# Kernel tuning notes

Measured on AMD Instinct MI355X. Metric: run time of the kernel, lower is better.

Reference implementation:

```python
import jax, jax.numpy as jnp
import numpy as np

B, T, HID = 2, 2048, 2048
NH, NKV = 16, 8
NOPE, ROPE = 128, 64
HD = NOPE + ROPE  # 192
VD = 128
KV_RANK, Q_RANK = 512, 1536
EPS = 1e-6
THETA = 10000.0
GROUPS = NH // NKV


def rmsnorm(x, w):
    var = jnp.mean(x * x, axis=-1, keepdims=True)
    return x * jax.lax.rsqrt(var + EPS) * w


def rope_cos_sin(seq_len, dtype):
    inv_freq = 1.0 / (THETA ** (jnp.arange(0, ROPE, 2, dtype=jnp.float32) / ROPE))
    t = jnp.arange(seq_len, dtype=jnp.float32)
    freqs = jnp.outer(t, inv_freq)
    emb = jnp.concatenate([freqs, freqs], axis=-1)  # [T, ROPE]
    return jnp.cos(emb).astype(dtype)[None, :, None, :], jnp.sin(emb).astype(dtype)[None, :, None, :]


def rotate_half(x):
    x1, x2 = x[..., : x.shape[-1] // 2], x[..., x.shape[-1] // 2 :]
    return jnp.concatenate([-x2, x1], axis=-1)


def setup_inputs() -> dict:
    key = jax.random.key(0)
    ks = jax.random.split(key, 7)
    s = 0.02
    return {
        "hidden_states": jax.random.normal(ks[0], (B, T, HID), jnp.float32),
        "q_a_w": jax.random.normal(ks[1], (HID, Q_RANK), jnp.float32) * s,
        "q_a_ln_w": jnp.ones((Q_RANK,), jnp.float32),
        "q_b_w": jax.random.normal(ks[2], (Q_RANK, NH * HD), jnp.float32) * s,
        "kv_a_w": jax.random.normal(ks[3], (HID, KV_RANK + NKV * ROPE), jnp.float32) * s,
        "kv_a_ln_w": jnp.ones((KV_RANK,), jnp.float32),
        "kv_b_w": jax.random.normal(ks[4], (KV_RANK, NKV * (NOPE + VD)), jnp.float32) * s,
        "o_w": jax.random.normal(ks[5], (NH * VD, HID), jnp.float32) * s,
    }


def reference(hidden_states, q_a_w, q_a_ln_w, q_b_w, kv_a_w, kv_a_ln_w, kv_b_w, o_w):
    x = hidden_states
    # Q low-rank path: a_proj -> RMSNorm -> b_proj
    q = rmsnorm(x @ q_a_w, q_a_ln_w) @ q_b_w
    q = q.reshape(B, T, NH, HD)
    q_nope, q_rope = q[..., :NOPE], q[..., NOPE:]
    # KV low-rank + decoupled rope key
    kv_raw = x @ kv_a_w
    kv_latent = rmsnorm(kv_raw[..., :KV_RANK], kv_a_ln_w)
    k_rope = kv_raw[..., KV_RANK:].reshape(B, T, NKV, ROPE)
    kv = (kv_latent @ kv_b_w).reshape(B, T, NKV, NOPE + VD)
    k_nope, v = kv[..., :NOPE], kv[..., NOPE:]
    # partial RoPE on rope slice only
    cos, sin = rope_cos_sin(T, x.dtype)
    q_rope = q_rope * cos + rotate_half(q_rope) * sin
    k_rope = k_rope * cos + rotate_half(k_rope) * sin
    q_full = jnp.concatenate([q_nope, q_rope], axis=-1)  # [B,T,NH,HD]
    k_full = jnp.concatenate([k_nope, k_rope], axis=-1)  # [B,T,NKV,HD]
    # GQA expansion (repeat_interleave over head dim)
    k_full = jnp.repeat(k_full, GROUPS, axis=2)  # [B,T,NH,HD]
    v_full = jnp.repeat(v, GROUPS, axis=2)       # [B,T,NH,VD]
    scale = HD ** -0.5
    scores = jnp.einsum("bqhd,bkhd->bhqk", q_full, k_full) * scale
    probs = jax.nn.softmax(scores, axis=-1)
    attn = jnp.einsum("bhqk,bkhd->bqhd", probs, v_full)
    out = attn.reshape(B, T, NH * VD) @ o_w
    return out
```

## Files before the change

kernel.cpp:

```cpp
#include <hip/hip_runtime.h>

using u16 = unsigned short;
using u32 = unsigned int;

typedef float f32x4 __attribute__((ext_vector_type(4)));
typedef __bf16 bf16x8 __attribute__((ext_vector_type(8)));
typedef u16 u16x8 __attribute__((ext_vector_type(8)));

__device__ __forceinline__ u16 f2bf(float f){
  u32 u = __builtin_bit_cast(u32, f);
  u32 r = (u + 0x7fffu + ((u >> 16) & 1u)) >> 16;
  return (u16)r;
}
__device__ __forceinline__ float bf2f(u16 h){
  u32 u = ((u32)h) << 16;
  return __builtin_bit_cast(float, u);
}
__device__ __forceinline__ void gl2lds16(const void* g, void* l){
  __builtin_amdgcn_global_load_lds((const __attribute__((address_space(1))) u32*)g,
                                   (__attribute__((address_space(3))) u32*)l, 16, 0, 0);
}
__device__ __forceinline__ int swz24(int ck, int r){ return (ck & 24) | ((ck ^ r) & 7); }

__global__ __launch_bounds__(256) void cvt_f32_bf16(const float* __restrict__ in,
                                                    u16* __restrict__ out, long n){
  long i = ((long)blockIdx.x*256 + threadIdx.x)*4;
  if (i >= n) return;
  float4 v = *(const float4*)(in + i);
  u16 o[4] = { f2bf(v.x), f2bf(v.y), f2bf(v.z), f2bf(v.w) };
  *(ushort4*)(out + i) = *(ushort4*)o;
}

__global__ __launch_bounds__(256) void transpose_w(const float* __restrict__ in,
                                                   u16* __restrict__ out, int K, int N){
  __shared__ float tile[32][33];
  int n0 = blockIdx.x*32, k0 = blockIdx.y*32;
  int tx = threadIdx.x, ty = threadIdx.y;
  for (int i = ty; i < 32; i += 8)
    tile[i][tx] = in[(size_t)(k0+i)*N + n0+tx];
  __syncthreads();
  for (int i = ty; i < 32; i += 8)
    out[(size_t)(n0+i)*K + k0+tx] = f2bf(tile[tx][i]);
}

__global__ __launch_bounds__(256) void rope_tables(float* __restrict__ cosT, float* __restrict__ sinT){
  int idx = blockIdx.x*256 + threadIdx.x;
  int t = idx >> 5, d = idx & 31;
  double inv = pow(10000.0, -(double)d / 32.0);
  double a = (double)t * inv;
  cosT[idx] = (float)cos(a);
  sinT[idx] = (float)sin(a);
}

template<int OUT_BF16>
__global__ __launch_bounds__(256) void gemm_bt(const u16* __restrict__ A,
                                               const u16* __restrict__ Bt,
                                               void* __restrict__ Cout,
                                               int M, int N, int K, float cscale){
  __shared__ u16 As[128*32];
  __shared__ u16 Bs[128*32];
  const int tid = threadIdx.x, lane = tid & 63, wave = tid >> 6;
  const int m0 = blockIdx.y*128, n0 = blockIdx.x*128;
  const int wm = (wave >> 1)*64, wn = (wave & 1)*64;
  const int g = lane >> 4, lr = lane & 15;
  f32x4 acc[4][4] = {};
  const int sr = (wave*2)*16 + (lane >> 2);
  const int sc = (lane & 3)*8;
  for (int k0 = 0; k0 < K; k0 += 32){
    __syncthreads();
    #pragma unroll
    for (int i = 0; i < 2; i++){
      int c = wave*2 + i;
      int r = sr + i*16;
      gl2lds16(A  + (size_t)(m0+r)*K + k0 + sc, (char*)As + c*1024);
      gl2lds16(Bt + (size_t)(n0+r)*K + k0 + sc, (char*)Bs + c*1024);
    }
    __syncthreads();
    bf16x8 af[4], bfr[4];
    #pragma unroll
    for (int mi = 0; mi < 4; mi++) af[mi]  = *reinterpret_cast<const bf16x8*>(&As[(wm+mi*16+lr)*32 + g*8]);
    #pragma unroll
    for (int ni = 0; ni < 4; ni++) bfr[ni] = *reinterpret_cast<const bf16x8*>(&Bs[(wn+ni*16+lr)*32 + g*8]);
    #pragma unroll
    for (int mi = 0; mi < 4; mi++)
      #pragma unroll
      for (int ni = 0; ni < 4; ni++)
        acc[mi][ni] = __builtin_amdgcn_mfma_f32_16x16x32_bf16(af[mi], bfr[ni], acc[mi][ni], 0,0,0);
  }
  #pragma unroll
  for (int mi = 0; mi < 4; mi++)
    #pragma unroll
    for (int ni = 0; ni < 4; ni++)
      #pragma unroll
      for (int r = 0; r < 4; r++){
        int row = m0 + wm + mi*16 + g*4 + r;
        int col = n0 + wn + ni*16 + lr;
        float v = acc[mi][ni][r];
        if (OUT_BF16) ((u16*)Cout)[(size_t)row*N + col] = f2bf(v*cscale);
        else          ((float*)Cout)[(size_t)row*N + col] = v;
      }
}

__global__ __launch_bounds__(256) void rmsnorm_kernel(const float* __restrict__ in,
                                                      const float* __restrict__ w,
                                                      u16* __restrict__ out, int ncols){
  int row = blockIdx.x;
  const float* x = in + (size_t)row*ncols;
  float ss = 0.f;
  for (int c = threadIdx.x; c < ncols; c += 256){ float v = x[c]; ss += v*v; }
  #pragma unroll
  for (int m = 1; m < 64; m <<= 1) ss += __shfl_xor(ss, m, 64);
  __shared__ float p[4];
  if ((threadIdx.x & 63) == 0) p[threadIdx.x >> 6] = ss;
  __syncthreads();
  float inv = rsqrtf((p[0]+p[1]+p[2]+p[3]) / (float)ncols + 1e-6f);
  u16* o = out + (size_t)row*ncols;
  for (int c = threadIdx.x; c < ncols; c += 256) o[c] = f2bf(x[c]*inv*w[c]);
}

__global__ __launch_bounds__(256) void kv_split_kernel(const float* __restrict__ kvraw,
                                                       const float* __restrict__ lnw,
                                                       const float* __restrict__ cosT,
                                                       const float* __restrict__ sinT,
                                                       u16* __restrict__ kvlat,
                                                       u16* __restrict__ Kf){
  int row = blockIdx.x;
  int t = row & 2047, b = row >> 11;
  const float* x = kvraw + (size_t)row*1024;
  float ss = 0.f;
  for (int c = threadIdx.x; c < 512; c += 256){ float v = x[c]; ss += v*v; }
  #pragma unroll
  for (int m = 1; m < 64; m <<= 1) ss += __shfl_xor(ss, m, 64);
  __shared__ float p[4];
  if ((threadIdx.x & 63) == 0) p[threadIdx.x >> 6] = ss;
  __syncthreads();
  float inv = rsqrtf((p[0]+p[1]+p[2]+p[3]) / 512.0f + 1e-6f);
  for (int c = threadIdx.x; c < 512; c += 256)
    kvlat[(size_t)row*512 + c] = f2bf(x[c]*inv*lnw[c]);
  int kh = threadIdx.x >> 5, dp = threadIdx.x & 31;
  float x1 = x[512 + kh*64 + dp], x2 = x[512 + kh*64 + dp + 32];
  float cv = cosT[t*32 + dp], sv = sinT[t*32 + dp];
  float o1 = x1*cv - x2*sv;
  float o2 = x2*cv + x1*sv;
  u16* kr = Kf + ((size_t)(b*8 + kh)*2048 + t)*192;
  int c1 = 128 + dp, c2 = 128 + dp + 32;
  kr[(swz24(c1 >> 3, t) << 3) | (c1 & 7)] = f2bf(o1);
  kr[(swz24(c2 >> 3, t) << 3) | (c2 & 7)] = f2bf(o2);
}

__global__ __launch_bounds__(256) void q_rope_kernel(u16* __restrict__ q,
                                                     const float* __restrict__ cosT,
                                                     const float* __restrict__ sinT){
  int idx = blockIdx.x*256 + threadIdx.x;
  int row = idx >> 9, rem = idx & 511;
  int h = rem >> 5, dp = rem & 31;
  int t = row & 2047;
  u16* pq = q + (size_t)row*3072 + h*192 + 128;
  float x1 = bf2f(pq[dp]), x2 = bf2f(pq[dp+32]);
  float cv = cosT[t*32 + dp], sv = sinT[t*32 + dp];
  pq[dp]    = f2bf(x1*cv - x2*sv);
  pq[dp+32] = f2bf(x2*cv + x1*sv);
}

__global__ __launch_bounds__(256) void knope_kernel(const u16* __restrict__ kv,
                                                    u16* __restrict__ Kf){
  int idx = blockIdx.x*256 + threadIdx.x;
  int row = idx >> 7, rem = idx & 127;
  int kh = rem >> 4, ck = rem & 15;
  int t = row & 2047, b = row >> 11;
  int ck2 = (ck & 8) | ((ck ^ t) & 7);
  uint4 v = *(const uint4*)(kv + (size_t)row*2048 + kh*256 + ck*8);
  *(uint4*)(Kf + ((size_t)(b*8 + kh)*2048 + t)*192 + ck2*8) = v;
}

__global__ __launch_bounds__(256) void v_transpose(const u16* __restrict__ kv,
                                                   u16* __restrict__ vT){
  int bid = blockIdx.x;
  int tt = bid & 31, kvh = (bid >> 5) & 7, b = bid >> 8;
  int t0 = tt*64;
  __shared__ u16 tile[64][136];
  int tid = threadIdx.x;
  #pragma unroll
  for (int i = 0; i < 4; i++){
    int c = tid + i*256;
    int r = c >> 4, ck = c & 15;
    const u16* src = kv + ((size_t)(b*2048 + t0 + r))*2048 + kvh*256 + 128 + ck*8;
    *(uint4*)&tile[r][ck*8] = *(const uint4*)src;
  }
  __syncthreads();
  #pragma unroll
  for (int i = 0; i < 4; i++){
    int c = tid + i*256;
    int vd = c >> 3, tc = c & 7;
    int stc = tc ^ (vd & 7);
    uint4 tv;
    u16* tp = (u16*)&tv;
    #pragma unroll
    for (int j = 0; j < 8; j++) tp[j] = tile[tc*8 + j][vd];
    *(uint4*)(vT + ((size_t)(b*8 + kvh)*128 + vd)*2048 + t0 + stc*8) = tv;
  }
}

__global__ __launch_bounds__(256, 2) void attn_kernel(const u16* __restrict__ Q,
                                                      const u16* __restrict__ Kf,
                                                      const u16* __restrict__ Vt,
                                                      u16* __restrict__ Oa){
  constexpr int T = 2048;
  constexpr int NT = T/64;
  __shared__ u16 Ks[64*192];
  __shared__ u16 Vs[2][128*64];
  __shared__ u16 Ps[4][2048];
  const int tid = threadIdx.x, lane = tid & 63, wave = tid >> 6;
  const int g = lane >> 4, lr = lane & 15;

  const int wg = blockIdx.x;
  const int role = (wg & 7)*64 + (wg >> 3);
  const int grp = role >> 5;
  const int b = grp >> 3, kvh = grp & 7;
  const int within = role & 31;
  const int h = kvh*2 + (within >> 4);
  const int q0 = (within & 15)*128 + wave*32;

  bf16x8 aq[2][6];
  #pragma unroll
  for (int qg = 0; qg < 2; qg++){
    const u16* qrow = Q + ((size_t)b*T + q0 + qg*16 + lr)*3072 + h*192;
    #pragma unroll
    for (int kc = 0; kc < 6; kc++)
      aq[qg][kc] = *reinterpret_cast<const bf16x8*>(qrow + kc*32 + g*8);
  }
  const u16* Kbase = Kf + (size_t)(b*8 + kvh)*T*192;
  const u16* Vbase = Vt + (size_t)(b*8 + kvh)*128*T;

  u16x8 onesb_u = {};
  #pragma unroll
  for (int j = 0; j < 8; j++) onesb_u[j] = (lr == 0) ? (u16)0x3F80 : (u16)0;
  const bf16x8 ones_b = __builtin_bit_cast(bf16x8, onesb_u);

  f32x4 ovb[2][8] = {};
  float mrow[2][4] = {{-1e30f,-1e30f,-1e30f,-1e30f},{-1e30f,-1e30f,-1e30f,-1e30f}};
  float lp[2][4] = {};

  auto stageK = [&](int kt){
    const u16* ksrc = Kbase + (size_t)kt*12288 + wave*3072 + lane*8;
    #pragma unroll
    for (int i = 0; i < 6; i++)
      gl2lds16(ksrc + i*512, (char*)Ks + (wave*6 + i)*1024);
  };
  auto stageV = [&](int kt, int buf){
    #pragma unroll
    for (int i = 0; i < 4; i++){
      int c = wave*4 + i;
      const u16* vsrc = Vbase + (size_t)(c*8 + (lane >> 3))*T + kt*64 + (lane & 7)*8;
      gl2lds16(vsrc, (char*)(&Vs[0][0]) + buf*16384 + c*1024);
    }
  };

  stageK(0);
  stageV(0, 0);
  __syncthreads();

  int buf = 0;
  for (int kt = 0; kt < NT; kt++){
    const bool notlast = (kt + 1 < NT);

    if (notlast) stageV(kt + 1, buf ^ 1);

    f32x4 s[2][4];
    __builtin_amdgcn_s_setprio(1);
    #pragma unroll
    for (int nb = 0; nb < 4; nb++){
      const int row = nb*16 + lr;
      f32x4 a0 = {0.f,0.f,0.f,0.f}, a1 = {0.f,0.f,0.f,0.f};
      #pragma unroll
      for (int kc = 0; kc < 6; kc++){
        int ckl = swz24(kc*4 + g, row);
        bf16x8 kf = *reinterpret_cast<const bf16x8*>(&Ks[row*192 + ckl*8]);
        a0 = __builtin_amdgcn_mfma_f32_16x16x32_bf16(aq[0][kc], kf, a0, 0,0,0);
        a1 = __builtin_amdgcn_mfma_f32_16x16x32_bf16(aq[1][kc], kf, a1, 0,0,0);
      }
      s[0][nb] = a0; s[1][nb] = a1;
    }
    __builtin_amdgcn_s_setprio(0);

    asm volatile("s_waitcnt lgkmcnt(0)" ::: "memory");
    __builtin_amdgcn_s_barrier();
    __builtin_amdgcn_sched_barrier(0);
    if (notlast) stageK(kt + 1);

    #pragma unroll
    for (int qg = 0; qg < 2; qg++){
      float tmax[4];
      #pragma unroll
      for (int r = 0; r < 4; r++){
        float v = fmaxf(fmaxf(s[qg][0][r], s[qg][1][r]), fmaxf(s[qg][2][r], s[qg][3][r]));
        v = fmaxf(v, __shfl_xor(v, 1, 64));
        v = fmaxf(v, __shfl_xor(v, 2, 64));
        v = fmaxf(v, __shfl_xor(v, 4, 64));
        v = fmaxf(v, __shfl_xor(v, 8, 64));
        tmax[r] = v;
      }
      int ok = (tmax[0] <= mrow[qg][0] + 8.f) & (tmax[1] <= mrow[qg][1] + 8.f) &
               (tmax[2] <= mrow[qg][2] + 8.f) & (tmax[3] <= mrow[qg][3] + 8.f);
      if (!__all(ok)){
        #pragma unroll
        for (int r = 0; r < 4; r++){
          float mn = fmaxf(mrow[qg][r], tmax[r]);
          float corr = __expf(mrow[qg][r] - mn);
          mrow[qg][r] = mn;
          lp[qg][r] *= corr;
          #pragma unroll
          for (int vb = 0; vb < 8; vb++) ovb[qg][vb][r] *= corr;
        }
      }
      #pragma unroll
      for (int nb = 0; nb < 4; nb++)
        #pragma unroll
        for (int r = 0; r < 4; r++){
          float pv = __expf(s[qg][nb][r] - mrow[qg][r]);
          int prow = g*4 + r, col = nb*16 + lr;
          int ck = (col >> 3) ^ (prow & 7);
          Ps[wave][qg*1024 + prow*64 + ck*8 + (col & 7)] = f2bf(pv);
        }
    }

    asm volatile("s_waitcnt lgkmcnt(0)" ::: "memory");
    __builtin_amdgcn_sched_barrier(0);

    bf16x8 ap[2][2];
    #pragma unroll
    for (int qg = 0; qg < 2; qg++)
      #pragma unroll
      for (int k2 = 0; k2 < 2; k2++){
        int ck = (k2*4 + g) ^ (lr & 7);
        ap[qg][k2] = *reinterpret_cast<const bf16x8*>(&Ps[wave][qg*1024 + lr*64 + ck*8]);
      }
    #pragma unroll
    for (int qg = 0; qg < 2; qg++){
      f32x4 ts = {0.f,0.f,0.f,0.f};
      ts = __builtin_amdgcn_mfma_f32_16x16x32_bf16(ap[qg][0], ones_b, ts, 0,0,0);
      ts = __builtin_amdgcn_mfma_f32_16x16x32_bf16(ap[qg][1], ones_b, ts, 0,0,0);
      #pragma unroll
      for (int r = 0; r < 4; r++) lp[qg][r] += ts[r];
    }
    __builtin_amdgcn_s_setprio(1);
    #pragma unroll
    for (int vb = 0; vb < 8; vb++)
      #pragma unroll
      for (int k2 = 0; k2 < 2; k2++){
        int vd = vb*16 + lr;
        int ck = (k2*4 + g) ^ (vd & 7);
        bf16x8 bv = *reinterpret_cast<const bf16x8*>(&Vs[buf][vd*64 + ck*8]);
        ovb[0][vb] = __builtin_amdgcn_mfma_f32_16x16x32_bf16(ap[0][k2], bv, ovb[0][vb], 0,0,0);
        ovb[1][vb] = __builtin_amdgcn_mfma_f32_16x16x32_bf16(ap[1][k2], bv, ovb[1][vb], 0,0,0);
      }
    __builtin_amdgcn_s_setprio(0);

    if (notlast) __syncthreads();
    buf ^= 1;
  }

  #pragma unroll
  for (int qg = 0; qg < 2; qg++){
    float inv[4];
    #pragma unroll
    for (int r = 0; r < 4; r++){
      float sum = __shfl(lp[qg][r], lane & 48, 64);
      inv[r] = 1.0f / sum;
    }
    u16* obase = Oa + ((size_t)b*T + q0 + qg*16)*2048 + h*128;
    #pragma unroll
    for (int vb = 0; vb < 8; vb++)
      #pragma unroll
      for (int r = 0; r < 4; r++)
        obase[(size_t)(g*4 + r)*2048 + vb*16 + lr] = f2bf(ovb[qg][vb][r]*inv[r]);
  }
}

extern "C" void kernel_launch(void* const* d_in, const int* in_sizes, int n_in,
                              void* d_out, int out_size, void* d_ws, size_t ws_size,
                              hipStream_t stream){
  const float* hs      = (const float*)d_in[0];
  const float* q_a_w   = (const float*)d_in[1];
  const float* q_a_ln  = (const float*)d_in[2];
  const float* q_b_w   = (const float*)d_in[3];
  const float* kv_a_w  = (const float*)d_in[4];
  const float* kv_a_ln = (const float*)d_in[5];
  const float* kv_b_w  = (const float*)d_in[6];
  const float* o_w     = (const float*)d_in[7];

  char* ws = (char*)d_ws;
  size_t off = 0;
  auto alloc = [&](size_t bytes){ void* p = ws + off; off += bytes; return p; };
  u16*  Wqa   = (u16*)alloc(1536ull*2048*2);
  u16*  Wqb   = (u16*)alloc(3072ull*1536*2);
  u16*  Wkva  = (u16*)alloc(1024ull*2048*2);
  u16*  Wkvb  = (u16*)alloc(2048ull*512*2);
  u16*  Wo    = (u16*)alloc(2048ull*2048*2);
  u16*  XB    = (u16*)alloc(4096ull*2048*2);
  char* R2    = (char*)alloc(4096ull*1536*4);
  char* R3    = (char*)alloc(4096ull*1024*4);
  u16*  Qlat  = (u16*)alloc(4096ull*1536*2);
  u16*  KVlat = (u16*)alloc(4096ull*512*2);
  u16*  Kf    = (u16*)alloc(2ull*8*2048*192*2);
  u16*  Vt    = (u16*)alloc(2ull*8*128*2048*2);
  float* cosT = (float*)alloc(2048ull*32*4);
  float* sinT = (float*)alloc(2048ull*32*4);
  (void)ws_size; (void)in_sizes; (void)n_in; (void)out_size;

  const float qscale = 0.07216878364870322f;

  cvt_f32_bf16<<<8192, 256, 0, stream>>>(hs, XB, 4096ll*2048);
  transpose_w<<<dim3(1536/32, 2048/32), dim3(32,8), 0, stream>>>(q_a_w,  Wqa,  2048, 1536);
  transpose_w<<<dim3(3072/32, 1536/32), dim3(32,8), 0, stream>>>(q_b_w,  Wqb,  1536, 3072);
  transpose_w<<<dim3(1024/32, 2048/32), dim3(32,8), 0, stream>>>(kv_a_w, Wkva, 2048, 1024);
  transpose_w<<<dim3(2048/32,  512/32), dim3(32,8), 0, stream>>>(kv_b_w, Wkvb,  512, 2048);
  transpose_w<<<dim3(2048/32, 2048/32), dim3(32,8), 0, stream>>>(o_w,    Wo,   2048, 2048);
  rope_tables<<<256, 256, 0, stream>>>(cosT, sinT);

  gemm_bt<0><<<dim3(12, 32), 256, 0, stream>>>(XB, Wqa,  (float*)R2, 4096, 1536, 2048, 1.0f);
  gemm_bt<0><<<dim3( 8, 32), 256, 0, stream>>>(XB, Wkva, (float*)R3, 4096, 1024, 2048, 1.0f);
  rmsnorm_kernel<<<4096, 256, 0, stream>>>((const float*)R2, q_a_ln, Qlat, 1536);
  kv_split_kernel<<<4096, 256, 0, stream>>>((const float*)R3, kv_a_ln, cosT, sinT, KVlat, Kf);
  gemm_bt<1><<<dim3(24, 32), 256, 0, stream>>>(Qlat, Wqb, (u16*)R2, 4096, 3072, 1536, qscale);
  q_rope_kernel<<<8192, 256, 0, stream>>>((u16*)R2, cosT, sinT);
  gemm_bt<1><<<dim3(16, 32), 256, 0, stream>>>(KVlat, Wkvb, (u16*)R3, 4096, 2048, 512, 1.0f);
  knope_kernel<<<2048, 256, 0, stream>>>((const u16*)R3, Kf);
  v_transpose<<<512, 256, 0, stream>>>((const u16*)R3, Vt);
  attn_kernel<<<512, 256, 0, stream>>>((const u16*)R2, Kf, Vt, XB);
  gemm_bt<0><<<dim3(16, 32), 256, 0, stream>>>(XB, Wo, (float*)d_out, 4096, 2048, 2048, 1.0f);
}
```

Before: 423.8 us.

## Fuse Q/KV down-projections and keep attention probabilities in registers

Wkva is laid out right after Wqa so the two down-projection GEMMs over the same input run as one GEMM with N=2560, and the rmsnorm and kv_split kernels now read strided rows of that output. The attention kernel computes S transposed (K as the A operand), so each lane holds whole score columns. Probabilities are then packed to bf16 in registers and fed straight into 16x16x16 MFMAs for the PV product, with no LDS round trip. Row max and sum use cross-lane shuffles instead of the ones-vector MFMA. The V tile loses its double buffer to cut LDS use and allow 3 blocks per CU. The cost is that the V load is no longer overlapped with compute, and extra barriers are added.

```diff
diff --git a/kernel.cpp b/kernel.cpp
--- a/kernel.cpp
+++ b/kernel.cpp
@@ -5,7 +5,7 @@
 
 typedef float f32x4 __attribute__((ext_vector_type(4)));
 typedef __bf16 bf16x8 __attribute__((ext_vector_type(8)));
-typedef u16 u16x8 __attribute__((ext_vector_type(8)));
+typedef u32 u32x2 __attribute__((ext_vector_type(2)));
 
 __device__ __forceinline__ u16 f2bf(float f){
   u32 u = __builtin_bit_cast(u32, f);
@@ -21,6 +21,12 @@
                                    (__attribute__((address_space(3))) u32*)l, 16, 0, 0);
 }
 __device__ __forceinline__ int swz24(int ck, int r){ return (ck & 24) | ((ck ^ r) & 7); }
+__device__ __forceinline__ u32 cvtpk_bf16(float a, float b){
+  u32 r; asm("v_cvt_pk_bf16_f32 %0, %1, %2" : "=v"(r) : "v"(a), "v"(b)); return r;
+}
+__device__ __forceinline__ void mfma16(f32x4& acc, u32x2 a, u32x2 b){
+  asm("v_mfma_f32_16x16x16_bf16 %0, %1, %2, %0" : "+v"(acc) : "v"(a), "v"(b));
+}
 
 __global__ __launch_bounds__(256) void cvt_f32_bf16(const float* __restrict__ in,
                                                     u16* __restrict__ out, long n){
@@ -103,9 +109,9 @@
 
 __global__ __launch_bounds__(256) void rmsnorm_kernel(const float* __restrict__ in,
                                                       const float* __restrict__ w,
-                                                      u16* __restrict__ out, int ncols){
+                                                      u16* __restrict__ out, int ncols, int instride){
   int row = blockIdx.x;
-  const float* x = in + (size_t)row*ncols;
+  const float* x = in + (size_t)row*instride;
   float ss = 0.f;
   for (int c = threadIdx.x; c < ncols; c += 256){ float v = x[c]; ss += v*v; }
   #pragma unroll
@@ -126,7 +132,7 @@
                                                        u16* __restrict__ Kf){
   int row = blockIdx.x;
   int t = row & 2047, b = row >> 11;
-  const float* x = kvraw + (size_t)row*1024;
+  const float* x = kvraw + (size_t)row*2560 + 1536;
   float ss = 0.f;
   for (int c = threadIdx.x; c < 512; c += 256){ float v = x[c]; ss += v*v; }
   #pragma unroll
@@ -201,15 +207,14 @@
   }
 }
 
-__global__ __launch_bounds__(256, 2) void attn_kernel(const u16* __restrict__ Q,
+__global__ __launch_bounds__(256, 3) void attn_kernel(const u16* __restrict__ Q,
                                                       const u16* __restrict__ Kf,
                                                       const u16* __restrict__ Vt,
                                                       u16* __restrict__ Oa){
   constexpr int T = 2048;
   constexpr int NT = T/64;
   __shared__ u16 Ks[64*192];
-  __shared__ u16 Vs[2][128*64];
-  __shared__ u16 Ps[4][2048];
+  __shared__ u16 Vs[128*64];
   const int tid = threadIdx.x, lane = tid & 63, wave = tid >> 6;
   const int g = lane >> 4, lr = lane & 15;
 
@@ -232,14 +237,9 @@
   const u16* Kbase = Kf + (size_t)(b*8 + kvh)*T*192;
   const u16* Vbase = Vt + (size_t)(b*8 + kvh)*128*T;
 
-  u16x8 onesb_u = {};
-  #pragma unroll
-  for (int j = 0; j < 8; j++) onesb_u[j] = (lr == 0) ? (u16)0x3F80 : (u16)0;
-  const bf16x8 ones_b = __builtin_bit_cast(bf16x8, onesb_u);
-
   f32x4 ovb[2][8] = {};
-  float mrow[2][4] = {{-1e30f,-1e30f,-1e30f,-1e30f},{-1e30f,-1e30f,-1e30f,-1e30f}};
-  float lp[2][4] = {};
+  float mq[2] = {-1e30f, -1e30f};
+  float lq[2] = {0.f, 0.f};
 
   auto stageK = [&](int kt){
     const u16* ksrc = Kbase + (size_t)kt*12288 + wave*3072 + lane*8;
@@ -247,24 +247,21 @@
     for (int i = 0; i < 6; i++)
       gl2lds16(ksrc + i*512, (char*)Ks + (wave*6 + i)*1024);
   };
-  auto stageV = [&](int kt, int buf){
+  auto stageV = [&](int kt){
     #pragma unroll
     for (int i = 0; i < 4; i++){
       int c = wave*4 + i;
       const u16* vsrc = Vbase + (size_t)(c*8 + (lane >> 3))*T + kt*64 + (lane & 7)*8;
-      gl2lds16(vsrc, (char*)(&Vs[0][0]) + buf*16384 + c*1024);
+      gl2lds16(vsrc, (char*)Vs + c*1024);
     }
   };
 
   stageK(0);
-  stageV(0, 0);
+  stageV(0);
   __syncthreads();
 
-  int buf = 0;
   for (int kt = 0; kt < NT; kt++){
     const bool notlast = (kt + 1 < NT);
-
-    if (notlast) stageV(kt + 1, buf ^ 1);
 
     f32x4 s[2][4];
     __builtin_amdgcn_s_setprio(1);
@@ -276,104 +273,91 @@
       for (int kc = 0; kc < 6; kc++){
         int ckl = swz24(kc*4 + g, row);
         bf16x8 kf = *reinterpret_cast<const bf16x8*>(&Ks[row*192 + ckl*8]);
-        a0 = __builtin_amdgcn_mfma_f32_16x16x32_bf16(aq[0][kc], kf, a0, 0,0,0);
-        a1 = __builtin_amdgcn_mfma_f32_16x16x32_bf16(aq[1][kc], kf, a1, 0,0,0);
+        a0 = __builtin_amdgcn_mfma_f32_16x16x32_bf16(kf, aq[0][kc], a0, 0,0,0);
+        a1 = __builtin_amdgcn_mfma_f32_16x16x32_bf16(kf, aq[1][kc], a1, 0,0,0);
       }
       s[0][nb] = a0; s[1][nb] = a1;
     }
     __builtin_amdgcn_s_setprio(0);
 
-    asm volatile("s_waitcnt lgkmcnt(0)" ::: "memory");
-    __builtin_amdgcn_s_barrier();
-    __builtin_amdgcn_sched_barrier(0);
+    __syncthreads();
     if (notlast) stageK(kt + 1);
 
+    u32 pk[2][4][2];
     #pragma unroll
     for (int qg = 0; qg < 2; qg++){
-      float tmax[4];
-      #pragma unroll
-      for (int r = 0; r < 4; r++){
-        float v = fmaxf(fmaxf(s[qg][0][r], s[qg][1][r]), fmaxf(s[qg][2][r], s[qg][3][r]));
-        v = fmaxf(v, __shfl_xor(v, 1, 64));
-        v = fmaxf(v, __shfl_xor(v, 2, 64));
-        v = fmaxf(v, __shfl_xor(v, 4, 64));
-        v = fmaxf(v, __shfl_xor(v, 8, 64));
-        tmax[r] = v;
-      }
-      int ok = (tmax[0] <= mrow[qg][0] + 8.f) & (tmax[1] <= mrow[qg][1] + 8.f) &
-               (tmax[2] <= mrow[qg][2] + 8.f) & (tmax[3] <= mrow[qg][3] + 8.f);
-      if (!__all(ok)){
+      float pm = s[qg][0][0];
+      #pragma unroll
+      for (int nb = 0; nb < 4; nb++)
+        #pragma unroll
+        for (int r = 0; r < 4; r++)
+          if (nb || r) pm = fmaxf(pm, s[qg][nb][r]);
+      pm = fmaxf(pm, __shfl_xor(pm, 16, 64));
+      pm = fmaxf(pm, __shfl_xor(pm, 32, 64));
+      if (!__all(pm <= mq[qg] + 8.f)){
+        float mn = fmaxf(mq[qg], pm);
+        float corr = __expf(mq[qg] - mn);
+        mq[qg] = mn;
+        lq[qg] *= corr;
         #pragma unroll
         for (int r = 0; r < 4; r++){
-          float mn = fmaxf(mrow[qg][r], tmax[r]);
-          float corr = __expf(mrow[qg][r] - mn);
-          mrow[qg][r] = mn;
-          lp[qg][r] *= corr;
+          float cr = __shfl(corr, (lane & 48) | (g*4 + r), 64);
           #pragma unroll
-          for (int vb = 0; vb < 8; vb++) ovb[qg][vb][r] *= corr;
+          for (int vb = 0; vb < 8; vb++) ovb[qg][vb][r] *= cr;
         }
       }
-      #pragma unroll
-      for (int nb = 0; nb < 4; nb++)
-        #pragma unroll
-        for (int r = 0; r < 4; r++){
-          float pv = __expf(s[qg][nb][r] - mrow[qg][r]);
-          int prow = g*4 + r, col = nb*16 + lr;
-          int ck = (col >> 3) ^ (prow & 7);
-          Ps[wave][qg*1024 + prow*64 + ck*8 + (col & 7)] = f2bf(pv);
-        }
-    }
-
-    asm volatile("s_waitcnt lgkmcnt(0)" ::: "memory");
-    __builtin_amdgcn_sched_barrier(0);
-
-    bf16x8 ap[2][2];
-    #pragma unroll
-    for (int qg = 0; qg < 2; qg++)
-      #pragma unroll
-      for (int k2 = 0; k2 < 2; k2++){
-        int ck = (k2*4 + g) ^ (lr & 7);
-        ap[qg][k2] = *reinterpret_cast<const bf16x8*>(&Ps[wave][qg*1024 + lr*64 + ck*8]);
+      float ls = 0.f;
+      #pragma unroll
+      for (int nb = 0; nb < 4; nb++){
+        float e0 = __expf(s[qg][nb][0] - mq[qg]);
+        float e1 = __expf(s[qg][nb][1] - mq[qg]);
+        float e2 = __expf(s[qg][nb][2] - mq[qg]);
+        float e3 = __expf(s[qg][nb][3] - mq[qg]);
+        ls += (e0 + e1) + (e2 + e3);
+        pk[qg][nb][0] = cvtpk_bf16(e0, e1);
+        pk[qg][nb][1] = cvtpk_bf16(e2, e3);
       }
-    #pragma unroll
-    for (int qg = 0; qg < 2; qg++){
-      f32x4 ts = {0.f,0.f,0.f,0.f};
-      ts = __builtin_amdgcn_mfma_f32_16x16x32_bf16(ap[qg][0], ones_b, ts, 0,0,0);
-      ts = __builtin_amdgcn_mfma_f32_16x16x32_bf16(ap[qg][1], ones_b, ts, 0,0,0);
-      #pragma unroll
-      for (int r = 0; r < 4; r++) lp[qg][r] += ts[r];
-    }
+      ls += __shfl_xor(ls, 16, 64);
+      ls += __shfl_xor(ls, 32, 64);
+      lq[qg] += ls;
+    }
+
     __builtin_amdgcn_s_setprio(1);
+    const int vsw = lr & 7;
+    #pragma unroll
+    for (int vb = 0; vb < 8; vb++){
+      const int vd = vb*16 + lr;
+      #pragma unroll
+      for (int nb = 0; nb < 4; nb++){
+        int ck = (nb*2 + (g >> 1)) ^ vsw;
+        u32x2 bv = *reinterpret_cast<const u32x2*>(&Vs[vd*64 + ck*8 + (g & 1)*4]);
+        u32x2 pa0; pa0.x = pk[0][nb][0]; pa0.y = pk[0][nb][1];
+        u32x2 pa1; pa1.x = pk[1][nb][0]; pa1.y = pk[1][nb][1];
+        mfma16(ovb[0][vb], pa0, bv);
+        mfma16(ovb[1][vb], pa1, bv);
+      }
+    }
+    __builtin_amdgcn_s_setprio(0);
+
+    if (notlast){
+      __syncthreads();
+      stageV(kt + 1);
+    }
+  }
+
+  #pragma unroll
+  for (int qg = 0; qg < 2; qg++){
+    float invq = 1.0f / lq[qg];
+    float inv_r[4];
+    #pragma unroll
+    for (int r = 0; r < 4; r++)
+      inv_r[r] = __shfl(invq, (lane & 48) | (g*4 + r), 64);
+    u16* obase = Oa + ((size_t)b*T + q0 + qg*16)*2048 + h*128;
     #pragma unroll
     for (int vb = 0; vb < 8; vb++)
       #pragma unroll
-      for (int k2 = 0; k2 < 2; k2++){
-        int vd = vb*16 + lr;
-        int ck = (k2*4 + g) ^ (vd & 7);
-        bf16x8 bv = *reinterpret_cast<const bf16x8*>(&Vs[buf][vd*64 + ck*8]);
-        ovb[0][vb] = __builtin_amdgcn_mfma_f32_16x16x32_bf16(ap[0][k2], bv, ovb[0][vb], 0,0,0);
-        ovb[1][vb] = __builtin_amdgcn_mfma_f32_16x16x32_bf16(ap[1][k2], bv, ovb[1][vb], 0,0,0);
-      }
-    __builtin_amdgcn_s_setprio(0);
-
-    if (notlast) __syncthreads();
-    buf ^= 1;
-  }
-
-  #pragma unroll
-  for (int qg = 0; qg < 2; qg++){
-    float inv[4];
-    #pragma unroll
-    for (int r = 0; r < 4; r++){
-      float sum = __shfl(lp[qg][r], lane & 48, 64);
-      inv[r] = 1.0f / sum;
-    }
-    u16* obase = Oa + ((size_t)b*T + q0 + qg*16)*2048 + h*128;
-    #pragma unroll
-    for (int vb = 0; vb < 8; vb++)
-      #pragma unroll
       for (int r = 0; r < 4; r++)
-        obase[(size_t)(g*4 + r)*2048 + vb*16 + lr] = f2bf(ovb[qg][vb][r]*inv[r]);
+        obase[(size_t)(g*4 + r)*2048 + vb*16 + lr] = f2bf(ovb[qg][vb][r]*inv_r[r]);
   }
 }
 
@@ -393,13 +377,12 @@
   size_t off = 0;
   auto alloc = [&](size_t bytes){ void* p = ws + off; off += bytes; return p; };
   u16*  Wqa   = (u16*)alloc(1536ull*2048*2);
+  u16*  Wkva  = (u16*)alloc(1024ull*2048*2);
   u16*  Wqb   = (u16*)alloc(3072ull*1536*2);
-  u16*  Wkva  = (u16*)alloc(1024ull*2048*2);
   u16*  Wkvb  = (u16*)alloc(2048ull*512*2);
   u16*  Wo    = (u16*)alloc(2048ull*2048*2);
   u16*  XB    = (u16*)alloc(4096ull*2048*2);
-  char* R2    = (char*)alloc(4096ull*1536*4);
-  char* R3    = (char*)alloc(4096ull*1024*4);
+  char* R23   = (char*)alloc(4096ull*2560*4);
   u16*  Qlat  = (u16*)alloc(4096ull*1536*2);
   u16*  KVlat = (u16*)alloc(4096ull*512*2);
   u16*  Kf    = (u16*)alloc(2ull*8*2048*192*2);
@@ -408,25 +391,27 @@
   float* sinT = (float*)alloc(2048ull*32*4);
   (void)ws_size; (void)in_sizes; (void)n_in; (void)out_size;
 
+  u16* QB  = (u16*)R23;
+  u16* KVB = (u16*)(R23 + 4096ull*3072*2);
+
   const float qscale = 0.07216878364870322f;
 
   cvt_f32_bf16<<<8192, 256, 0, stream>>>(hs, XB, 4096ll*2048);
   transpose_w<<<dim3(1536/32, 2048/32), dim3(32,8), 0, stream>>>(q_a_w,  Wqa,  2048, 1536);
+  transpose_w<<<dim3(1024/32, 2048/32), dim3(32,8), 0, stream>>>(kv_a_w, Wkva, 2048, 1024);
   transpose_w<<<dim3(3072/32, 1536/32), dim3(32,8), 0, stream>>>(q_b_w,  Wqb,  1536, 3072);
-  transpose_w<<<dim3(1024/32, 2048/32), dim3(32,8), 0, stream>>>(kv_a_w, Wkva, 2048, 1024);
   transpose_w<<<dim3(2048/32,  512/32), dim3(32,8), 0, stream>>>(kv_b_w, Wkvb,  512, 2048);
   transpose_w<<<dim3(2048/32, 2048/32), dim3(32,8), 0, stream>>>(o_w,    Wo,   2048, 2048);
   rope_tables<<<256, 256, 0, stream>>>(cosT, sinT);
 
-  gemm_bt<0><<<dim3(12, 32), 256, 0, stream>>>(XB, Wqa,  (float*)R2, 4096, 1536, 2048, 1.0f);
-  gemm_bt<0><<<dim3( 8, 32), 256, 0, stream>>>(XB, Wkva, (float*)R3, 4096, 1024, 2048, 1.0f);
-  rmsnorm_kernel<<<4096, 256, 0, stream>>>((const float*)R2, q_a_ln, Qlat, 1536);
-  kv_split_kernel<<<4096, 256, 0, stream>>>((const float*)R3, kv_a_ln, cosT, sinT, KVlat, Kf);
-  gemm_bt<1><<<dim3(24, 32), 256, 0, stream>>>(Qlat, Wqb, (u16*)R2, 4096, 3072, 1536, qscale);
-  q_rope_kernel<<<8192, 256, 0, stream>>>((u16*)R2, cosT, sinT);
-  gemm_bt<1><<<dim3(16, 32), 256, 0, stream>>>(KVlat, Wkvb, (u16*)R3, 4096, 2048, 512, 1.0f);
-  knope_kernel<<<2048, 256, 0, stream>>>((const u16*)R3, Kf);
-  v_transpose<<<512, 256, 0, stream>>>((const u16*)R3, Vt);
-  attn_kernel<<<512, 256, 0, stream>>>((const u16*)R2, Kf, Vt, XB);
+  gemm_bt<0><<<dim3(20, 32), 256, 0, stream>>>(XB, Wqa, (float*)R23, 4096, 2560, 2048, 1.0f);
+  rmsnorm_kernel<<<4096, 256, 0, stream>>>((const float*)R23, q_a_ln, Qlat, 1536, 2560);
+  kv_split_kernel<<<4096, 256, 0, stream>>>((const float*)R23, kv_a_ln, cosT, sinT, KVlat, Kf);
+  gemm_bt<1><<<dim3(24, 32), 256, 0, stream>>>(Qlat, Wqb, QB, 4096, 3072, 1536, qscale);
+  q_rope_kernel<<<8192, 256, 0, stream>>>(QB, cosT, sinT);
+  gemm_bt<1><<<dim3(16, 32), 256, 0, stream>>>(KVlat, Wkvb, KVB, 4096, 2048, 512, 1.0f);
+  knope_kernel<<<2048, 256, 0, stream>>>(KVB, Kf);
+  v_transpose<<<512, 256, 0, stream>>>(KVB, Vt);
+  attn_kernel<<<512, 256, 0, stream>>>(QB, Kf, Vt, XB);
   gemm_bt<0><<<dim3(16, 32), 256, 0, stream>>>(XB, Wo, (float*)d_out, 4096, 2048, 2048, 1.0f);
 }
```

Result: no change. 416.4 us (-1.7%).
